# Performance work log

Hardware: AMD Instinct MI355X
Metric: run time of the kernel (lower is better)

## Reference

```python
import jax, jax.numpy as jnp
import numpy as np

E = 768
H = 8
EXP = 4
HEAD_D = E // H  # 96, also the post-softmax scaling factor


def _layernorm(x, g, b, eps=1e-5):
    mu = jnp.mean(x, axis=-1, keepdims=True)
    var = jnp.var(x, axis=-1, keepdims=True)
    return (x - mu) * jax.lax.rsqrt(var + eps) * g + b


def setup_inputs() -> dict:
    key = jax.random.key(0)
    ks = jax.random.split(key, 12)
    s = 0.02
    inp = {
        "x": jax.random.normal(ks[0], (8, 1024, E), dtype=jnp.float32),
        "ln1_g": jnp.ones((E,), jnp.float32),
        "ln1_b": jnp.zeros((E,), jnp.float32),
        "Wq": jax.random.normal(ks[1], (E, E), jnp.float32) * s,
        "bq": jnp.zeros((E,), jnp.float32),
        "Wk": jax.random.normal(ks[2], (E, E), jnp.float32) * s,
        "bk": jnp.zeros((E,), jnp.float32),
        "Wv": jax.random.normal(ks[3], (E, E), jnp.float32) * s,
        "bv": jnp.zeros((E,), jnp.float32),
        "Wo": jax.random.normal(ks[4], (E, E), jnp.float32) * s,
        "bo": jnp.zeros((E,), jnp.float32),
        "ln2_g": jnp.ones((E,), jnp.float32),
        "ln2_b": jnp.zeros((E,), jnp.float32),
        "W1": jax.random.normal(ks[5], (E, EXP * E), jnp.float32) * s,
        "b1": jnp.zeros((EXP * E,), jnp.float32),
        "W2": jax.random.normal(ks[6], (EXP * E, E), jnp.float32) * s,
        "b2": jnp.zeros((E,), jnp.float32),
    }
    return inp


def reference(x, ln1_g, ln1_b, Wq, bq, Wk, bk, Wv, bv, Wo, bo,
              ln2_g, ln2_b, W1, b1, W2, b2):
    B, N, _ = x.shape
    # --- sub_block_1: LN -> MHA (post-softmax scaling) -> residual ---
    h = _layernorm(x, ln1_g, ln1_b)
    q = (h @ Wq + bq).reshape(B, N, H, HEAD_D).transpose(0, 2, 1, 3)
    k = (h @ Wk + bk).reshape(B, N, H, HEAD_D).transpose(0, 2, 1, 3)
    v = (h @ Wv + bv).reshape(B, N, H, HEAD_D).transpose(0, 2, 1, 3)
    energy = jnp.einsum('bhqd,bhkd->bhqk', q, k)  # NOTE: no pre-softmax scale
    att = jax.nn.softmax(energy, axis=-1) * HEAD_D  # quirky post-softmax scaling
    out = jnp.einsum('bhqk,bhkd->bhqd', att, v)
    out = out.transpose(0, 2, 1, 3).reshape(B, N, E)
    out = out @ Wo + bo
    x = x + out  # residual
    # --- sub_block_2: LN -> GELU-FFN (NO residual, faithful to source) ---
    h = _layernorm(x, ln2_g, ln2_b)
    h = jax.nn.gelu(h @ W1 + b1, approximate=False)
    return h @ W2 + b2
```

## Files before the change

kernel.cpp:

```cpp
#include <hip/hip_runtime.h>
#include <hip/hip_bf16.h>
#include <math.h>

#define DI __device__ __forceinline__

typedef __attribute__((ext_vector_type(8))) __bf16 bf16x8;
typedef __attribute__((ext_vector_type(8))) short short8;
typedef __attribute__((ext_vector_type(4))) float f32x4;
typedef __attribute__((ext_vector_type(4))) int int4v;
typedef __attribute__((ext_vector_type(4))) unsigned short ushort4v;

DI short f2bfn(float f) {
  __bf16 b = (__bf16)f;
  short s;
  __builtin_memcpy(&s, &b, 2);
  return s;
}

DI float erf_fast(float x) {
  const float ax = fabsf(x);
  const float t = __builtin_amdgcn_rcpf(1.0f + 0.3275911f * ax);
  float p = 1.061405429f;
  p = p * t - 1.453152027f;
  p = p * t + 1.421413741f;
  p = p * t - 0.284496736f;
  p = p * t + 0.254829592f;
  p = p * t;
  const float r = 1.0f - p * __expf(-ax * ax);
  return copysignf(r, x);
}

DI void gload_lds16(const void* g, void* l) {
  __builtin_amdgcn_global_load_lds(
      (const __attribute__((address_space(1))) void*)g,
      (__attribute__((address_space(3))) void*)l, 16, 0, 0);
}

__global__ __launch_bounds__(256) void transpose_cvt(
    const float* __restrict__ in, short* __restrict__ out, int K, int N)
{
  __shared__ float tile[32][33];
  const int tx = threadIdx.x & 31, ty = threadIdx.x >> 5;
  const int n0 = blockIdx.x * 32, k0 = blockIdx.y * 32;
#pragma unroll
  for (int p = 0; p < 4; ++p)
    tile[ty + p * 8][tx] = in[(size_t)(k0 + ty + p * 8) * N + n0 + tx];
  __syncthreads();
#pragma unroll
  for (int p = 0; p < 4; ++p)
    out[(size_t)(n0 + ty + p * 8) * K + k0 + tx] = f2bfn(tile[tx][ty + p * 8]);
}

__global__ __launch_bounds__(256) void v_transpose(
    const short* __restrict__ qkv, short* __restrict__ vT)
{
  __shared__ short tile[64][98];
  const int t = threadIdx.x;
  const int bh = blockIdx.x, nt = blockIdx.y;
  const int b = bh >> 3, h = bh & 7;
  const size_t gbase = (size_t)(b * 1024 + nt * 64) * 2304 + 1536 + h * 96;
#pragma unroll
  for (int i = 0; i < 3; ++i) {
    const int p = i * 256 + t;
    const int row = p / 12, cb = p % 12;
    const short8 v = *(const short8*)(qkv + gbase + (size_t)row * 2304 + cb * 8);
#pragma unroll
    for (int j = 0; j < 4; ++j) {
      unsigned pk = (unsigned)(unsigned short)v[2 * j] |
                    ((unsigned)(unsigned short)v[2 * j + 1] << 16);
      *(unsigned*)&tile[row][cb * 8 + 2 * j] = pk;
    }
  }
  __syncthreads();
#pragma unroll
  for (int i = 0; i < 3; ++i) {
    const int p = i * 256 + t;
    const int d = p >> 3, cb = p & 7;
    short8 o;
#pragma unroll
    for (int j = 0; j < 8; ++j) o[j] = tile[cb * 8 + j][d];
    *(short8*)(vT + ((size_t)bh * 96 + d) * 1024 + nt * 64 + cb * 8) = o;
  }
}

__global__ __launch_bounds__(256) void ln_rows(
    const float* __restrict__ x, const float* __restrict__ gw,
    const float* __restrict__ bw, unsigned short* __restrict__ out)
{
  const int wv = threadIdx.x >> 6, ln = threadIdx.x & 63;
  const size_t row = (size_t)blockIdx.x * 4 + wv;
  const float* xr = x + row * 768;
  float4 v[3];
  float s = 0.f, sq = 0.f;
#pragma unroll
  for (int i = 0; i < 3; ++i) {
    v[i] = *(const float4*)(xr + i * 256 + ln * 4);
    s  += v[i].x + v[i].y + v[i].z + v[i].w;
    sq += v[i].x * v[i].x + v[i].y * v[i].y + v[i].z * v[i].z + v[i].w * v[i].w;
  }
#pragma unroll
  for (int msk = 1; msk < 64; msk <<= 1) {
    s  += __shfl_xor(s, msk);
    sq += __shfl_xor(sq, msk);
  }
  const float mean = s * (1.f / 768.f);
  const float var  = sq * (1.f / 768.f) - mean * mean;
  const float rstd = rsqrtf(var + 1e-5f);
#pragma unroll
  for (int i = 0; i < 3; ++i) {
    const int c = i * 256 + ln * 4;
    const float vals[4] = {v[i].x, v[i].y, v[i].z, v[i].w};
    ushort4v o;
#pragma unroll
    for (int j = 0; j < 4; ++j)
      o[j] = (unsigned short)f2bfn((vals[j] - mean) * rstd * gw[c + j] + bw[c + j]);
    *(ushort4v*)(out + row * 768 + c) = o;
  }
}

enum { EPI_BF16 = 0, EPI_F32_RES = 1, EPI_BF16_GELU = 2, EPI_F32 = 3 };

template <int MODE, int BM, int BK, int MW>
__global__ __launch_bounds__(256, MW) void gemm_bt(
    const short* __restrict__ A,
    const short* __restrict__ Bt,
    const float* __restrict__ bias,
    const float* __restrict__ resid,
    void* __restrict__ Cout, int ldc,
    int Ntiles, int K)
{
  constexpr int NCHUNK = BK / 8;
  constexpr int CMASK = NCHUNK - 1;
  constexpr int ABYTES = BM * BK * 2;
  constexpr int STAGE_BYTES = (BM + 128) * BK * 2;
  constexpr int NLA = BM * BK / 8 / 256;
  constexpr int NLB = 128 * BK / 8 / 256;
  constexpr int LOADS = NLA + NLB;
  constexpr int MR = BM / 32;
  constexpr int NKK = BK / 32;
  constexpr int SMEM = 2 * STAGE_BYTES > 4 * 4352 ? 2 * STAGE_BYTES : 4 * 4352;
  __shared__ __align__(16) char smem[SMEM];
  const int t = threadIdx.x;
  const int wv = t >> 6, ln = t & 63;
  const int g = ln >> 4, r = ln & 15;
  const int sw = ((int)blockIdx.x & 7) * ((int)gridDim.x >> 3) + ((int)blockIdx.x >> 3);
  const int bm = sw / Ntiles, bn = sw % Ntiles;
  const int wr = wv >> 1, wc = wv & 1;
  f32x4 acc[MR][4] = {};

  const char* aptr[NLA];
  const char* bptr[NLB];
#pragma unroll
  for (int q = 0; q < NLA; ++q) {
    const int p = q * 256 + t;
    const int row = p / NCHUNK, c = (p & CMASK) ^ (row & CMASK);
    aptr[q] = (const char*)(A + (size_t)(bm * BM + row) * K + c * 8);
  }
#pragma unroll
  for (int q = 0; q < NLB; ++q) {
    const int p = q * 256 + t;
    const int row = p / NCHUNK, c = (p & CMASK) ^ (row & CMASK);
    bptr[q] = (const char*)(Bt + (size_t)(bn * 128 + row) * K + c * 8);
  }

  auto stage = [&](int buf) {
    char* as = smem + buf * STAGE_BYTES;
    char* bs = as + ABYTES;
#pragma unroll
    for (int q = 0; q < NLA; ++q) {
      gload_lds16(aptr[q], as + q * 4096 + wv * 1024);
      aptr[q] += BK * 2;
    }
#pragma unroll
    for (int q = 0; q < NLB; ++q) {
      gload_lds16(bptr[q], bs + q * 4096 + wv * 1024);
      bptr[q] += BK * 2;
    }
  };

  const int nk = K / BK;
  stage(0);
  stage(1);
  int cur = 0;
  for (int kt = 0; kt < nk; ++kt) {
    if (kt + 1 < nk)
      asm volatile("s_waitcnt vmcnt(%0)\n\ts_barrier" :: "n"(LOADS) : "memory");
    else
      asm volatile("s_waitcnt vmcnt(0)\n\ts_barrier" ::: "memory");
    const short* as = (const short*)(smem + cur * STAGE_BYTES);
    const short* bs = as + ABYTES / 2;
    bf16x8 af[MR][NKK], bfr[4][NKK];
#pragma unroll
    for (int m = 0; m < MR; ++m) {
      const int row = wr * (BM / 2) + m * 16 + r;
#pragma unroll
      for (int kk = 0; kk < NKK; ++kk)
        af[m][kk] = *(const bf16x8*)(as + row * BK + (((kk * 4 + g) ^ (row & CMASK)) << 3));
    }
#pragma unroll
    for (int n = 0; n < 4; ++n) {
      const int row = wc * 64 + n * 16 + r;
#pragma unroll
      for (int kk = 0; kk < NKK; ++kk)
        bfr[n][kk] = *(const bf16x8*)(bs + row * BK + (((kk * 4 + g) ^ (row & CMASK)) << 3));
    }
#pragma unroll
    for (int kk = 0; kk < NKK; ++kk)
#pragma unroll
      for (int m = 0; m < MR; ++m)
#pragma unroll
        for (int n = 0; n < 4; ++n)
          acc[m][n] = __builtin_amdgcn_mfma_f32_16x16x32_bf16(af[m][kk], bfr[n][kk],
                                                              acc[m][n], 0, 0, 0);
    if (kt + 2 < nk) {
      asm volatile("s_waitcnt lgkmcnt(0)\n\ts_barrier" ::: "memory");
      stage(cur);
    }
    cur ^= 1;
  }
  __syncthreads();

  float* epi = (float*)(smem + wv * 4352);
  const int cq = (ln & 3) * 16;
  const int lr = ln >> 2;
  const int c0 = bn * 128 + wc * 64 + cq;
  f32x4 bv[4];
#pragma unroll
  for (int j = 0; j < 4; ++j) bv[j] = *(const f32x4*)(bias + c0 + j * 4);

#pragma unroll
  for (int m = 0; m < MR; ++m) {
#pragma unroll
    for (int n = 0; n < 4; ++n)
#pragma unroll
      for (int q = 0; q < 4; ++q)
        epi[(g * 4 + q) * 68 + n * 16 + r] = acc[m][n][q];
    const size_t grow = (size_t)(bm * BM + wr * (BM / 2) + m * 16 + lr);
    float vals[16];
#pragma unroll
    for (int j = 0; j < 4; ++j) {
      const f32x4 vv = *(const f32x4*)(epi + lr * 68 + cq + j * 4);
#pragma unroll
      for (int e = 0; e < 4; ++e) vals[j * 4 + e] = vv[e] + bv[j][e];
    }
    if constexpr (MODE == EPI_F32_RES) {
#pragma unroll
      for (int j = 0; j < 4; ++j) {
        const f32x4 rv = *(const f32x4*)(resid + grow * ldc + c0 + j * 4);
#pragma unroll
        for (int e = 0; e < 4; ++e) vals[j * 4 + e] += rv[e];
      }
    }
    if constexpr (MODE == EPI_BF16_GELU) {
#pragma unroll
      for (int j = 0; j < 16; ++j)
        vals[j] = 0.5f * vals[j] * (1.0f + erf_fast(vals[j] * 0.70710678118654752f));
    }
    if constexpr (MODE == EPI_F32 || MODE == EPI_F32_RES) {
      float* op = (float*)Cout + grow * ldc + c0;
#pragma unroll
      for (int j = 0; j < 4; ++j) {
        f32x4 ov;
#pragma unroll
        for (int e = 0; e < 4; ++e) ov[e] = vals[j * 4 + e];
        *(f32x4*)(op + j * 4) = ov;
      }
    } else {
      unsigned short* op = (unsigned short*)Cout + grow * ldc + c0;
#pragma unroll
      for (int hhalf = 0; hhalf < 2; ++hhalf) {
        short8 ov;
#pragma unroll
        for (int e = 0; e < 8; ++e) ov[e] = f2bfn(vals[hhalf * 8 + e]);
        *(short8*)(op + hhalf * 8) = ov;
      }
    }
  }
}

__global__ __launch_bounds__(256, 2) void attn_fwd(
    const short* __restrict__ qkv, const short* __restrict__ vT,
    unsigned short* __restrict__ ab)
{
  __shared__ short Ks[2][64 * 128];
  __shared__ short Vs[2][96 * 64];
  __shared__ short Ps[4][2][16 * 64];
  const int t = threadIdx.x, wv = t >> 6, ln = t & 63;
  const int g = ln >> 4, r = ln & 15;
  const int bid = ((int)blockIdx.x & 7) * 64 + ((int)blockIdx.x >> 3);
  const int bh = bid >> 3, qt = bid & 7;
  const int b = bh >> 3, h = bh & 7;

  bf16x8 qf[2][3];
#pragma unroll
  for (int u = 0; u < 2; ++u) {
    const size_t rowq = (size_t)(b * 1024 + qt * 128 + wv * 32 + u * 16 + r);
#pragma unroll
    for (int kd = 0; kd < 3; ++kd)
      qf[u][kd] = *(const bf16x8*)(qkv + rowq * 2304 + h * 96 + kd * 32 + g * 8);
  }

  size_t offK[4];
#pragma unroll
  for (int i = 0; i < 4; ++i) {
    const int p = i * 256 + t;
    const int row = p >> 4, cb = p & 15, cbs = cb ^ (row & 7);
    offK[i] = (size_t)row * 2304 + 768 + h * 96 + (cbs << 3);
  }
  size_t offV[3];
#pragma unroll
  for (int i = 0; i < 3; ++i) {
    const int p = i * 256 + t;
    const int row = p >> 3, cb = p & 7, cbs = cb ^ (row & 7);
    offV[i] = ((size_t)bh * 96 + row) * 1024 + (cbs << 3);
  }
  const short* qb = qkv + (size_t)b * 1024 * 2304;

  auto stageKV = [&](int buf, int kt) {
    const size_t kadd = (size_t)kt * 64 * 2304;
#pragma unroll
    for (int i = 0; i < 4; ++i)
      gload_lds16(qb + kadd + offK[i], (char*)Ks[buf] + i * 4096 + wv * 1024);
#pragma unroll
    for (int i = 0; i < 3; ++i)
      gload_lds16(vT + offV[i] + kt * 64, (char*)Vs[buf] + i * 4096 + wv * 1024);
  };

  f32x4 o[2][6] = {};
  float mr[2] = {-1e30f, -1e30f}, lr[2] = {0.f, 0.f};

  stageKV(0, 0);
  __syncthreads();
  int cur = 0;
  for (int kt = 0; kt < 16; ++kt) {
    if (kt < 15) stageKV(cur ^ 1, kt + 1);
    const short* ks = Ks[cur];
    const short* vs = Vs[cur];

    f32x4 s[2][4] = {};
    __builtin_amdgcn_s_setprio(1);
#pragma unroll
    for (int sub = 0; sub < 4; ++sub) {
      bf16x8 kf[3];
#pragma unroll
      for (int kd = 0; kd < 3; ++kd)
        kf[kd] = *(const bf16x8*)(
            ks + (sub * 16 + r) * 128 + (((kd * 4 + g) ^ (r & 7)) << 3));
#pragma unroll
      for (int u = 0; u < 2; ++u)
#pragma unroll
        for (int kd = 0; kd < 3; ++kd)
          s[u][sub] = __builtin_amdgcn_mfma_f32_16x16x32_bf16(kf[kd], qf[u][kd],
                                                              s[u][sub], 0, 0, 0);
    }
    __builtin_amdgcn_s_setprio(0);

#pragma unroll
    for (int u = 0; u < 2; ++u) {
      float tm = fmaxf(fmaxf(s[u][0][0], s[u][0][1]),
                       fmaxf(s[u][0][2], s[u][0][3]));
#pragma unroll
      for (int sub = 1; sub < 4; ++sub)
        tm = fmaxf(tm, fmaxf(fmaxf(s[u][sub][0], s[u][sub][1]),
                             fmaxf(s[u][sub][2], s[u][sub][3])));
      tm = fmaxf(tm, __shfl_xor(tm, 16));
      tm = fmaxf(tm, __shfl_xor(tm, 32));

      if (__any(tm > mr[u] + 8.f)) {
        const float mnew = fmaxf(mr[u], tm);
        const float sc = __expf(mr[u] - mnew);
        lr[u] *= sc;
        mr[u] = mnew;
        float scr[4];
#pragma unroll
        for (int reg = 0; reg < 4; ++reg)
          scr[reg] = __shfl(sc, (ln & 48) | (g * 4 + reg));
#pragma unroll
        for (int nd = 0; nd < 6; ++nd)
#pragma unroll
          for (int reg = 0; reg < 4; ++reg) o[u][nd][reg] *= scr[reg];
      }

      float tsum = 0.f;
#pragma unroll
      for (int sub = 0; sub < 4; ++sub) {
        float p0 = __expf(s[u][sub][0] - mr[u]);
        float p1 = __expf(s[u][sub][1] - mr[u]);
        float p2 = __expf(s[u][sub][2] - mr[u]);
        float p3 = __expf(s[u][sub][3] - mr[u]);
        tsum += (p0 + p1) + (p2 + p3);
        ushort4v pk;
        pk[0] = (unsigned short)f2bfn(p0);
        pk[1] = (unsigned short)f2bfn(p1);
        pk[2] = (unsigned short)f2bfn(p2);
        pk[3] = (unsigned short)f2bfn(p3);
        const int c8 = (sub * 4 + g) ^ ((r & 7) << 1);
        *(ushort4v*)((char*)Ps[wv][u] + r * 128 + c8 * 8) = pk;
      }
      tsum += __shfl_xor(tsum, 16);
      tsum += __shfl_xor(tsum, 32);
      lr[u] += tsum;
    }

    bf16x8 pf[2][2];
#pragma unroll
    for (int u = 0; u < 2; ++u)
#pragma unroll
      for (int kk = 0; kk < 2; ++kk)
        pf[u][kk] = *(const bf16x8*)(
            Ps[wv][u] + r * 64 + (((kk * 4 + g) ^ (r & 7)) << 3));
    __builtin_amdgcn_s_setprio(1);
#pragma unroll
    for (int nd = 0; nd < 6; ++nd) {
      bf16x8 vf[2];
#pragma unroll
      for (int kk = 0; kk < 2; ++kk)
        vf[kk] = *(const bf16x8*)(
            vs + (nd * 16 + r) * 64 + (((kk * 4 + g) ^ (r & 7)) << 3));
#pragma unroll
      for (int u = 0; u < 2; ++u)
#pragma unroll
        for (int kk = 0; kk < 2; ++kk)
          o[u][nd] = __builtin_amdgcn_mfma_f32_16x16x32_bf16(pf[u][kk], vf[kk],
                                                             o[u][nd], 0, 0, 0);
    }
    __builtin_amdgcn_s_setprio(0);

    __syncthreads();
    cur ^= 1;
  }

#pragma unroll
  for (int u = 0; u < 2; ++u) {
    float linv[4];
#pragma unroll
    for (int reg = 0; reg < 4; ++reg)
      linv[reg] = 96.0f / __shfl(lr[u], (ln & 48) | (g * 4 + reg));
#pragma unroll
    for (int reg = 0; reg < 4; ++reg) {
      const size_t row = (size_t)(b * 1024 + qt * 128 + wv * 32 + u * 16 + g * 4 + reg);
#pragma unroll
      for (int nd = 0; nd < 6; ++nd)
        ab[row * 768 + h * 96 + nd * 16 + r] =
            (unsigned short)f2bfn(o[u][nd][reg] * linv[reg]);
    }
  }
}

extern "C" void kernel_launch(void* const* d_in, const int* in_sizes, int n_in,
                              void* d_out, int out_size, void* d_ws, size_t ws_size,
                              hipStream_t stream)
{
  const float* x    = (const float*)d_in[0];
  const float* ln1g = (const float*)d_in[1];
  const float* ln1b = (const float*)d_in[2];
  const float* Wq   = (const float*)d_in[3];
  const float* bq   = (const float*)d_in[4];
  const float* Wk   = (const float*)d_in[5];
  const float* bk   = (const float*)d_in[6];
  const float* Wv   = (const float*)d_in[7];
  const float* bv   = (const float*)d_in[8];
  const float* Wo   = (const float*)d_in[9];
  const float* bo   = (const float*)d_in[10];
  const float* ln2g = (const float*)d_in[11];
  const float* ln2b = (const float*)d_in[12];
  const float* W1   = (const float*)d_in[13];
  const float* b1   = (const float*)d_in[14];
  const float* W2   = (const float*)d_in[15];
  const float* b2   = (const float*)d_in[16];

  char* ws = (char*)d_ws;
  size_t off = 0;
  short* Wtqkv = (short*)(ws + off); off += (size_t)2304 * 768 * 2;
  short* Wto   = (short*)(ws + off); off += (size_t)768 * 768 * 2;
  short* Wt1   = (short*)(ws + off); off += (size_t)3072 * 768 * 2;
  short* Wt2   = (short*)(ws + off); off += (size_t)768 * 3072 * 2;
  float* bqkv  = (float*)(ws + off); off += 16384;
  short* hb    = (short*)(ws + off); off += (size_t)8192 * 768 * 2;
  short* qkv   = (short*)(ws + off); off += (size_t)8192 * 2304 * 2;
  short* h2b   = (short*)(ws + off); off += (size_t)8192 * 768 * 2;
  short* f1 = hb;
  short* ab = hb;
  short* vT = h2b;
  float* x1 = (float*)d_out;

  transpose_cvt<<<dim3(24, 24), 256, 0, stream>>>(Wq, Wtqkv, 768, 768);
  transpose_cvt<<<dim3(24, 24), 256, 0, stream>>>(Wk, Wtqkv + (size_t)768 * 768, 768, 768);
  transpose_cvt<<<dim3(24, 24), 256, 0, stream>>>(Wv, Wtqkv + (size_t)1536 * 768, 768, 768);
  transpose_cvt<<<dim3(24, 24), 256, 0, stream>>>(Wo, Wto, 768, 768);
  transpose_cvt<<<dim3(96, 24), 256, 0, stream>>>(W1, Wt1, 768, 3072);
  transpose_cvt<<<dim3(24, 96), 256, 0, stream>>>(W2, Wt2, 3072, 768);
  hipMemcpyAsync(bqkv,        bq, 768 * sizeof(float), hipMemcpyDeviceToDevice, stream);
  hipMemcpyAsync(bqkv + 768,  bk, 768 * sizeof(float), hipMemcpyDeviceToDevice, stream);
  hipMemcpyAsync(bqkv + 1536, bv, 768 * sizeof(float), hipMemcpyDeviceToDevice, stream);

  ln_rows<<<2048, 256, 0, stream>>>(x, ln1g, ln1b, (unsigned short*)hb);
  gemm_bt<EPI_BF16, 128, 32, 4><<<64 * 18, 256, 0, stream>>>(hb, Wtqkv, bqkv, nullptr, qkv, 2304, 18, 768);
  v_transpose<<<dim3(64, 16), 256, 0, stream>>>(qkv, vT);
  attn_fwd<<<512, 256, 0, stream>>>(qkv, vT, (unsigned short*)ab);
  gemm_bt<EPI_F32_RES, 64, 64, 3><<<128 * 6, 256, 0, stream>>>(ab, Wto, bo, x, x1, 768, 6, 768);

  ln_rows<<<2048, 256, 0, stream>>>(x1, ln2g, ln2b, (unsigned short*)h2b);
  gemm_bt<EPI_BF16_GELU, 128, 32, 4><<<64 * 24, 256, 0, stream>>>(h2b, Wt1, b1, nullptr, f1, 3072, 24, 768);
  gemm_bt<EPI_F32, 64, 64, 3><<<128 * 6, 256, 0, stream>>>(f1, Wt2, b2, nullptr, (float*)d_out, 768, 6, 3072);
}
```

Measured before the change: 262.9 us.

## Fuse V transpose into QKV GEMM epilogue and merge weight prep launches

The QKV GEMM gets a new epilogue mode: tiles covering the V columns write bias-added bf16 values straight into the transposed vT layout, so the separate v_transpose kernel and its reread of the V slice go away. The six weight transpose/convert launches and three bias memcpys are merged into one weight_prep kernel, which removes launch overhead. The cost is a branchy epilogue whose vT stores are 16-byte chunks scattered across rows, and some extra control flow in the prep kernel.

```diff
diff --git a/kernel.cpp b/kernel.cpp
--- a/kernel.cpp
+++ b/kernel.cpp
@@ -36,12 +36,41 @@
       (__attribute__((address_space(3))) void*)l, 16, 0, 0);
 }
 
-__global__ __launch_bounds__(256) void transpose_cvt(
-    const float* __restrict__ in, short* __restrict__ out, int K, int N)
+__global__ __launch_bounds__(256) void weight_prep(
+    const float* __restrict__ Wq, const float* __restrict__ Wk,
+    const float* __restrict__ Wv, const float* __restrict__ Wo,
+    const float* __restrict__ W1, const float* __restrict__ W2,
+    const float* __restrict__ bq, const float* __restrict__ bk,
+    const float* __restrict__ bv,
+    short* __restrict__ Wtqkv, short* __restrict__ Wto,
+    short* __restrict__ Wt1, short* __restrict__ Wt2,
+    float* __restrict__ bqkv)
 {
+  const int id = blockIdx.x, t = threadIdx.x;
+  if (id >= 6912) {
+    const int j = id - 6912;
+    const float* src = j == 0 ? bq : (j == 1 ? bk : bv);
+    for (int e = t; e < 768; e += 256) bqkv[j * 768 + e] = src[e];
+    return;
+  }
+  const float* in;
+  short* out;
+  int K, N, bx, by;
+  if (id < 2304) {
+    const int w = id / 576, r2 = id % 576;
+    bx = r2 % 24; by = r2 / 24; K = 768; N = 768;
+    in = (w == 0) ? Wq : (w == 1) ? Wk : (w == 2) ? Wv : Wo;
+    out = (w < 3) ? Wtqkv + (size_t)w * 768 * 768 : Wto;
+  } else if (id < 4608) {
+    const int r2 = id - 2304;
+    bx = r2 % 96; by = r2 / 96; K = 768; N = 3072; in = W1; out = Wt1;
+  } else {
+    const int r2 = id - 4608;
+    bx = r2 % 24; by = r2 / 24; K = 3072; N = 768; in = W2; out = Wt2;
+  }
   __shared__ float tile[32][33];
-  const int tx = threadIdx.x & 31, ty = threadIdx.x >> 5;
-  const int n0 = blockIdx.x * 32, k0 = blockIdx.y * 32;
+  const int tx = t & 31, ty = t >> 5;
+  const int n0 = bx * 32, k0 = by * 32;
 #pragma unroll
   for (int p = 0; p < 4; ++p)
     tile[ty + p * 8][tx] = in[(size_t)(k0 + ty + p * 8) * N + n0 + tx];
@@ -49,38 +78,6 @@
 #pragma unroll
   for (int p = 0; p < 4; ++p)
     out[(size_t)(n0 + ty + p * 8) * K + k0 + tx] = f2bfn(tile[tx][ty + p * 8]);
-}
-
-__global__ __launch_bounds__(256) void v_transpose(
-    const short* __restrict__ qkv, short* __restrict__ vT)
-{
-  __shared__ short tile[64][98];
-  const int t = threadIdx.x;
-  const int bh = blockIdx.x, nt = blockIdx.y;
-  const int b = bh >> 3, h = bh & 7;
-  const size_t gbase = (size_t)(b * 1024 + nt * 64) * 2304 + 1536 + h * 96;
-#pragma unroll
-  for (int i = 0; i < 3; ++i) {
-    const int p = i * 256 + t;
-    const int row = p / 12, cb = p % 12;
-    const short8 v = *(const short8*)(qkv + gbase + (size_t)row * 2304 + cb * 8);
-#pragma unroll
-    for (int j = 0; j < 4; ++j) {
-      unsigned pk = (unsigned)(unsigned short)v[2 * j] |
-                    ((unsigned)(unsigned short)v[2 * j + 1] << 16);
-      *(unsigned*)&tile[row][cb * 8 + 2 * j] = pk;
-    }
-  }
-  __syncthreads();
-#pragma unroll
-  for (int i = 0; i < 3; ++i) {
-    const int p = i * 256 + t;
-    const int d = p >> 3, cb = p & 7;
-    short8 o;
-#pragma unroll
-    for (int j = 0; j < 8; ++j) o[j] = tile[cb * 8 + j][d];
-    *(short8*)(vT + ((size_t)bh * 96 + d) * 1024 + nt * 64 + cb * 8) = o;
-  }
 }
 
 __global__ __launch_bounds__(256) void ln_rows(
@@ -118,7 +115,7 @@
   }
 }
 
-enum { EPI_BF16 = 0, EPI_F32_RES = 1, EPI_BF16_GELU = 2, EPI_F32 = 3 };
+enum { EPI_BF16 = 0, EPI_F32_RES = 1, EPI_BF16_GELU = 2, EPI_F32 = 3, EPI_QKV = 4 };
 
 template <int MODE, int BM, int BK, int MW>
 __global__ __launch_bounds__(256, MW) void gemm_bt(
@@ -126,8 +123,8 @@
     const short* __restrict__ Bt,
     const float* __restrict__ bias,
     const float* __restrict__ resid,
-    void* __restrict__ Cout, int ldc,
-    int Ntiles, int K)
+    void* __restrict__ Cout, short* __restrict__ vTout,
+    int ldc, int Ntiles, int K)
 {
   constexpr int NCHUNK = BK / 8;
   constexpr int CMASK = NCHUNK - 1;
@@ -221,6 +218,36 @@
   __syncthreads();
 
   float* epi = (float*)(smem + wv * 4352);
+
+  if constexpr (MODE == EPI_QKV) {
+    if (bn * 128 >= 1536) {
+      const int tc = ln;
+      const int cglob = bn * 128 + wc * 64 + tc;
+      const int cv = cglob - 1536;
+      const float bvs = bias[cglob];
+#pragma unroll
+      for (int m = 0; m < MR; ++m) {
+#pragma unroll
+        for (int n = 0; n < 4; ++n)
+#pragma unroll
+          for (int q = 0; q < 4; ++q)
+            epi[(g * 4 + q) * 68 + n * 16 + r] = acc[m][n][q];
+        float tv[16];
+#pragma unroll
+        for (int row = 0; row < 16; ++row) tv[row] = epi[row * 68 + tc] + bvs;
+        const int tokbase = bm * BM + wr * (BM / 2) + m * 16;
+        const int bb = tokbase >> 10, toff = tokbase & 1023;
+        short8 o0, o1;
+#pragma unroll
+        for (int e = 0; e < 8; ++e) { o0[e] = f2bfn(tv[e]); o1[e] = f2bfn(tv[e + 8]); }
+        short* dst = vTout + ((size_t)(bb * 768 + cv)) * 1024 + toff;
+        *(short8*)dst = o0;
+        *(short8*)(dst + 8) = o1;
+      }
+      return;
+    }
+  }
+
   const int cq = (ln & 3) * 16;
   const int lr = ln >> 2;
   const int c0 = bn * 128 + wc * 64 + cq;
@@ -484,23 +511,19 @@
   short* vT = h2b;
   float* x1 = (float*)d_out;
 
-  transpose_cvt<<<dim3(24, 24), 256, 0, stream>>>(Wq, Wtqkv, 768, 768);
-  transpose_cvt<<<dim3(24, 24), 256, 0, stream>>>(Wk, Wtqkv + (size_t)768 * 768, 768, 768);
-  transpose_cvt<<<dim3(24, 24), 256, 0, stream>>>(Wv, Wtqkv + (size_t)1536 * 768, 768, 768);
-  transpose_cvt<<<dim3(24, 24), 256, 0, stream>>>(Wo, Wto, 768, 768);
-  transpose_cvt<<<dim3(96, 24), 256, 0, stream>>>(W1, Wt1, 768, 3072);
-  transpose_cvt<<<dim3(24, 96), 256, 0, stream>>>(W2, Wt2, 3072, 768);
-  hipMemcpyAsync(bqkv,        bq, 768 * sizeof(float), hipMemcpyDeviceToDevice, stream);
-  hipMemcpyAsync(bqkv + 768,  bk, 768 * sizeof(float), hipMemcpyDeviceToDevice, stream);
-  hipMemcpyAsync(bqkv + 1536, bv, 768 * sizeof(float), hipMemcpyDeviceToDevice, stream);
+  weight_prep<<<6915, 256, 0, stream>>>(Wq, Wk, Wv, Wo, W1, W2, bq, bk, bv,
+                                        Wtqkv, Wto, Wt1, Wt2, bqkv);
 
   ln_rows<<<2048, 256, 0, stream>>>(x, ln1g, ln1b, (unsigned short*)hb);
-  gemm_bt<EPI_BF16, 128, 32, 4><<<64 * 18, 256, 0, stream>>>(hb, Wtqkv, bqkv, nullptr, qkv, 2304, 18, 768);
-  v_transpose<<<dim3(64, 16), 256, 0, stream>>>(qkv, vT);
+  gemm_bt<EPI_QKV, 128, 32, 4><<<64 * 18, 256, 0, stream>>>(
+      hb, Wtqkv, bqkv, nullptr, qkv, vT, 2304, 18, 768);
   attn_fwd<<<512, 256, 0, stream>>>(qkv, vT, (unsigned short*)ab);
-  gemm_bt<EPI_F32_RES, 64, 64, 3><<<128 * 6, 256, 0, stream>>>(ab, Wto, bo, x, x1, 768, 6, 768);
+  gemm_bt<EPI_F32_RES, 64, 64, 3><<<128 * 6, 256, 0, stream>>>(
+      ab, Wto, bo, x, x1, nullptr, 768, 6, 768);
 
   ln_rows<<<2048, 256, 0, stream>>>(x1, ln2g, ln2b, (unsigned short*)h2b);
-  gemm_bt<EPI_BF16_GELU, 128, 32, 4><<<64 * 24, 256, 0, stream>>>(h2b, Wt1, b1, nullptr, f1, 3072, 24, 768);
-  gemm_bt<EPI_F32, 64, 64, 3><<<128 * 6, 256, 0, stream>>>(f1, Wt2, b2, nullptr, (float*)d_out, 768, 6, 3072);
-}
+  gemm_bt<EPI_BF16_GELU, 128, 32, 4><<<64 * 24, 256, 0, stream>>>(
+      h2b, Wt1, b1, nullptr, f1, nullptr, 3072, 24, 768);
+  gemm_bt<EPI_F32, 64, 64, 3><<<128 * 6, 256, 0, stream>>>(
+      f1, Wt2, b2, nullptr, (float*)d_out, nullptr, 768, 6, 3072);
+}
```

Result: faster. 242.3 us (-7.8%).
